# Kernel optimization log

Measured on AMD Instinct MI355X. Metric: run time of the kernel, lower is better.

The kernel has to match this reference:

```python
import jax, jax.numpy as jnp
import numpy as np

EPS = 1e-5  # torch GroupNorm default


def setup_inputs() -> dict:
    key = jax.random.key(0)
    ks = jax.random.split(key, 6)
    C = 256
    B, F, H, W = 1, 8, 32, 32
    scale = 1.0 / np.sqrt(C)  # keep logits well-scaled
    return {
        "x": jax.random.normal(ks[0], (B, C, F, H, W), dtype=jnp.float32),
        "gn_w": jnp.ones((C,), jnp.float32),
        "gn_b": jnp.zeros((C,), jnp.float32),
        "qw": jax.random.normal(ks[1], (C, C), jnp.float32) * scale,
        "qb": jnp.zeros((C,), jnp.float32),
        "kw": jax.random.normal(ks[2], (C, C), jnp.float32) * scale,
        "kb": jnp.zeros((C,), jnp.float32),
        "vw": jax.random.normal(ks[3], (C, C), jnp.float32) * scale,
        "vb": jnp.zeros((C,), jnp.float32),
        "ow": jax.random.normal(ks[4], (C, C), jnp.float32) * scale,
        "ob": jnp.zeros((C,), jnp.float32),
    }


def reference(x, gn_w, gn_b, qw, qb, kw, kb, vw, vb, ow, ob):
    B, C, F, H, W = x.shape
    N = F * H * W
    # GroupNorm(1, C): normalize over (C,F,H,W) per sample, per-channel affine
    mean = jnp.mean(x, axis=(1, 2, 3, 4), keepdims=True)
    var = jnp.var(x, axis=(1, 2, 3, 4), keepdims=True)
    xn = (x - mean) * jax.lax.rsqrt(var + EPS)
    xn = xn * gn_w[None, :, None, None, None] + gn_b[None, :, None, None, None]
    xf = xn.reshape(B, C, N)  # [B, C, N]
    # 1x1x1 Conv3d == channel matmul
    q = jnp.einsum('oc,bcn->bon', qw, xf) + qb[None, :, None]
    k = jnp.einsum('oc,bcn->bon', kw, xf) + kb[None, :, None]
    v = jnp.einsum('oc,bcn->bon', vw, xf) + vb[None, :, None]
    # scores[b, n_q, n_k] = q^T k, scaled by C^-0.5
    scores = jnp.einsum('bcn,bcm->bnm', q, k) * (C ** -0.5)
    weights = jax.nn.softmax(scores, axis=-1)  # over keys
    # attention[b, c, n_q] = sum_m v[b,c,m] * weights[b,n_q,m]
    att = jnp.einsum('bcm,bnm->bcn', v, weights)
    att = jnp.einsum('oc,bcn->bon', ow, att) + ob[None, :, None]
    return xn + att.reshape(B, C, F, H, W)
```

## Files before the change

### kernel.cpp

```cpp
#include <hip/hip_runtime.h>
#include <hip/hip_bf16.h>
#include <cstdint>

#define NSP 8192
#define CCH 256
#define KBLK 32
#define NSPLIT 8
#define KEYS_PER_SPLIT 1024
#define NTILES 32

typedef __attribute__((ext_vector_type(4))) float f32x4;
typedef __attribute__((ext_vector_type(16))) float f32x16;
typedef __attribute__((ext_vector_type(8))) short bf16x8;
typedef __attribute__((ext_vector_type(2))) unsigned int u32x2;

__device__ __forceinline__ ushort f2bf(float f) {
  union { float f; uint32_t u; } v; v.f = f;
  uint32_t r = (v.u + 0x7FFFu + ((v.u >> 16) & 1u)) >> 16;
  return (ushort)r;
}
__device__ __forceinline__ float bf2f(ushort u) {
  union { uint32_t u; float f; } v; v.u = ((uint32_t)u) << 16; return v.f;
}
__device__ __forceinline__ uint32_t pk2bf(float lo, float hi) {
  __hip_bfloat162 h = __float22bfloat162_rn({lo, hi});
  union { __hip_bfloat162 h; uint32_t u; } c; c.h = h; return c.u;
}

__device__ __forceinline__ void gload_lds16(const void* g, void* l) {
  auto gp = (const __attribute__((address_space(1))) uint32_t*)(uintptr_t)g;
  auto lp = (__attribute__((address_space(3))) uint32_t*)(uint32_t)(uintptr_t)l;
  __builtin_amdgcn_global_load_lds(gp, lp, 16, 0, 0);
}

__device__ __forceinline__ void perm32swap(uint32_t& a, uint32_t& b) {
#if __has_builtin(__builtin_amdgcn_permlane32_swap)
  u32x2 r = __builtin_amdgcn_permlane32_swap(a, b, false, false);
  a = r[0]; b = r[1];
#else
  uint32_t sa = __shfl_xor((int)a, 32), sb = __shfl_xor((int)b, 32);
  bool lo = (threadIdx.x & 63) < 32;
  uint32_t na = lo ? a : sb;
  uint32_t nb = lo ? sa : b;
  a = na; b = nb;
#endif
}

__global__ __launch_bounds__(256) void k_stats1(const float* __restrict__ x,
                                                float* __restrict__ part) {
  int t = threadIdx.x, b = blockIdx.x;
  float s = 0.f, ss = 0.f;
  const float4* x4 = (const float4*)x;
  for (int i = 0; i < 4; ++i) {
    float4 v = x4[(size_t)i * 131072 + b * 256 + t];
    s += v.x + v.y + v.z + v.w;
    ss += v.x * v.x + v.y * v.y + v.z * v.z + v.w * v.w;
  }
  for (int m = 1; m < 64; m <<= 1) { s += __shfl_xor(s, m); ss += __shfl_xor(ss, m); }
  __shared__ float ls[4], lss[4];
  int w = t >> 6, lane = t & 63;
  if (lane == 0) { ls[w] = s; lss[w] = ss; }
  __syncthreads();
  if (t == 0) {
    part[b * 2 + 0] = ls[0] + ls[1] + ls[2] + ls[3];
    part[b * 2 + 1] = lss[0] + lss[1] + lss[2] + lss[3];
  }
}

__global__ __launch_bounds__(256) void k_castw(const float* __restrict__ qw, const float* __restrict__ kw,
                                               const float* __restrict__ vw, const float* __restrict__ ow,
                                               ushort* __restrict__ wqkv, ushort* __restrict__ wo,
                                               const float* __restrict__ part, float* __restrict__ stat) {
  if (blockIdx.x == 1024) {
    int t = threadIdx.x;
    float s = 0.f, ss = 0.f;
    for (int i = t; i < 512; i += 256) { s += part[i * 2]; ss += part[i * 2 + 1]; }
    for (int m = 1; m < 64; m <<= 1) { s += __shfl_xor(s, m); ss += __shfl_xor(ss, m); }
    __shared__ float ls[4], lss[4];
    int w = t >> 6, lane = t & 63;
    if (lane == 0) { ls[w] = s; lss[w] = ss; }
    __syncthreads();
    if (t == 0) {
      float sum = ls[0] + ls[1] + ls[2] + ls[3];
      float ssum = lss[0] + lss[1] + lss[2] + lss[3];
      float mean = sum * (1.f / 2097152.f);
      float var = ssum * (1.f / 2097152.f) - mean * mean;
      stat[0] = mean;
      stat[1] = rsqrtf(var + 1e-5f);
    }
    return;
  }
  int idx = blockIdx.x * 256 + threadIdx.x;
  if (idx < 65536) wqkv[idx] = f2bf(qw[idx]);
  else if (idx < 131072) wqkv[idx] = f2bf(kw[idx - 65536]);
  else if (idx < 196608) wqkv[idx] = f2bf(vw[idx - 131072]);
  else wo[idx - 196608] = f2bf(ow[idx - 196608]);
}

__global__ __launch_bounds__(256) void k_norm_t(const float* __restrict__ x,
                                                const float* __restrict__ gw, const float* __restrict__ gb,
                                                const float* __restrict__ stat, ushort* __restrict__ xnT) {
  __shared__ float tile[64][66];
  int n0 = blockIdx.x * 64, c0 = blockIdx.y * 64;
  int t = threadIdx.x, colr = t & 63, rq = t >> 6;
  float mean = stat[0], rinv = stat[1];
  for (int rr = 0; rr < 16; ++rr) {
    int row = rr * 4 + rq;
    int c = c0 + row;
    float v = x[(size_t)c * NSP + n0 + colr];
    tile[row][colr] = (v - mean) * rinv * gw[c] + gb[c];
  }
  __syncthreads();
  for (int rr = 0; rr < 16; ++rr) {
    int rowW = rr * 4 + rq;
    xnT[(size_t)(n0 + rowW) * 256 + c0 + colr] = f2bf(tile[colr][rowW]);
  }
}

__global__ __launch_bounds__(256) void k_qkv(const ushort* __restrict__ xnT, const ushort* __restrict__ wqkv,
                                             const float* __restrict__ qb, const float* __restrict__ kb,
                                             const float* __restrict__ vb,
                                             ushort* __restrict__ qT, ushort* __restrict__ kT,
                                             ushort* __restrict__ v_tiles) {
  __shared__ ushort tile[64][80];
  int nb = blockIdx.x, ob = blockIdx.y;
  int w = threadIdx.x >> 6, lane = threadIdx.x & 63;
  int l16 = lane & 15, kgrp = lane >> 4;
  int n_row = nb * 64 + w * 16 + l16;
  bf16x8 a[8];
  const bf16x8* arow = (const bf16x8*)(xnT + (size_t)n_row * 256);
  for (int ks = 0; ks < 8; ++ks) a[ks] = arow[ks * 4 + kgrp];
  f32x4 acc[4];
  for (int ct = 0; ct < 4; ++ct) {
    int o = ob * 64 + ct * 16 + l16;
    const bf16x8* brow = (const bf16x8*)(wqkv + (size_t)o * 256);
    f32x4 c = {0.f, 0.f, 0.f, 0.f};
    for (int ks = 0; ks < 8; ++ks)
      c = __builtin_amdgcn_mfma_f32_16x16x32_bf16(a[ks], brow[ks * 4 + kgrp], c, 0, 0, 0);
    acc[ct] = c;
  }
  const float SCALE = 0.0625f * 1.44269504088896340736f;
  if (ob < 8) {
    for (int ct = 0; ct < 4; ++ct) {
      int o = ob * 64 + ct * 16 + l16;
      for (int r = 0; r < 4; ++r) {
        int n = nb * 64 + w * 16 + kgrp * 4 + r;
        float v = acc[ct][r];
        if (o < 256) qT[(size_t)n * 256 + o] = f2bf((v + qb[o]) * SCALE);
        else kT[(size_t)n * 256 + (o - 256)] = f2bf(v + kb[o - 256]);
      }
    }
  } else {
    for (int ct = 0; ct < 4; ++ct) {
      int o_l = ct * 16 + l16;
      for (int r = 0; r < 4; ++r) {
        int n_l = w * 16 + kgrp * 4 + r;
        tile[o_l][n_l] = f2bf(acc[ct][r] + vb[(ob - 8) * 64 + o_l]);
      }
    }
    __syncthreads();
    for (int j = 0; j < 2; ++j) {
      int idx = j * 256 + threadIdx.x;
      int tile_l = idx >> 8, slot = (idx >> 6) & 3, c_l = idx & 63;
      size_t off = (size_t)(nb * 2 + tile_l) * 8192 + slot * 2048 +
                   (size_t)((ob - 8) * 64 + c_l) * 8;
      *(uint4*)((char*)v_tiles + off * 2) = *(const uint4*)&tile[c_l][tile_l * 32 + slot * 8];
    }
  }
}

__global__ __launch_bounds__(512, 2) void k_attn(const ushort* __restrict__ qT, const ushort* __restrict__ kT,
                                                 const ushort* __restrict__ v_tiles,
                                                 ushort* __restrict__ Opart, float* __restrict__ mpart,
                                                 float* __restrict__ lpart) {
  __shared__ __align__(16) ushort SMEM[32768];
  ushort* k_lds = SMEM;
  ushort* v_lds = SMEM + 16384;

  int bid = blockIdx.x;
  int split = bid & 7, qblk = bid >> 3;
  int t = threadIdx.x, w = t >> 6, lane = t & 63;
  int l31 = lane & 31, lhi = lane >> 5, l7 = lane & 7;
  int q0w = qblk * 256 + w * 32;

  bf16x8 qf[16];
  {
    const char* qbase = (const char*)qT + (size_t)(q0w + l31) * 512;
#pragma unroll
    for (int cs = 0; cs < 16; ++cs)
      qf[cs] = *(const bf16x8*)(qbase + cs * 32 + lhi * 16);
  }

  f32x16 acc[8] = {};
  float m_r = -1e30f, l_p = 0.f;
  bf16x8 pf0, pf1;

  const char* kT_b = (const char*)kT + (size_t)split * KEYS_PER_SPLIT * 512;
  const char* v_b = (const char*)v_tiles + (size_t)split * KEYS_PER_SPLIT * 512;

  auto STAGE_K = [&](int tt) {
    const char* ksrc = kT_b + (size_t)tt * KBLK * 512;
    char* kdst = (char*)(k_lds + (tt & 1) * 8192) + w * 2048;
#pragma unroll
    for (int i = 0; i < 2; ++i) {
      int keyloc = w * 4 + i * 2 + lhi;
      int srcoff = keyloc * 512 + ((l31 ^ (keyloc & 7)) << 4);
      gload_lds16(ksrc + srcoff, kdst + i * 1024);
    }
  };
  auto STAGE_V = [&](int tt) {
    char* vdst = (char*)(v_lds + (tt & 1) * 8192) + w * 2048;
    const char* vsrc = v_b + (size_t)tt * 16384 + w * 2048;
#pragma unroll
    for (int i = 0; i < 2; ++i)
      gload_lds16(vsrc + i * 1024 + lane * 16, vdst + i * 1024);
  };

  auto SOFTMAX_PACK = [&](f32x16& S0) {
    float x0 = fmaxf(S0[0], S0[1]), x1 = fmaxf(S0[2], S0[3]);
    float x2 = fmaxf(S0[4], S0[5]), x3 = fmaxf(S0[6], S0[7]);
    float x4 = fmaxf(S0[8], S0[9]), x5 = fmaxf(S0[10], S0[11]);
    float x6 = fmaxf(S0[12], S0[13]), x7 = fmaxf(S0[14], S0[15]);
    float pm = fmaxf(fmaxf(fmaxf(x0, x1), fmaxf(x2, x3)),
                     fmaxf(fmaxf(x4, x5), fmaxf(x6, x7)));
    pm = fmaxf(pm, __shfl_xor(pm, 32));
    if (!__all(pm <= m_r + 8.f)) {
      float mn = fmaxf(m_r, pm);
      float alpha = __builtin_amdgcn_exp2f(m_r - mn);
      m_r = mn;
      l_p *= alpha;
#pragma unroll
      for (int cb = 0; cb < 8; ++cb)
#pragma unroll
        for (int r = 0; r < 16; ++r) acc[cb][r] *= alpha;
    }
    {
      float t0s = 0.f, t1s = 0.f, t2s = 0.f, t3s = 0.f;
#pragma unroll
      for (int r = 0; r < 16; ++r) {
        S0[r] = __builtin_amdgcn_exp2f(S0[r] - m_r);
        if (r < 4) t0s += S0[r];
        else if (r < 8) t1s += S0[r];
        else if (r < 12) t2s += S0[r];
        else t3s += S0[r];
      }
      l_p += (t0s + t1s) + (t2s + t3s);
    }
    union { uint32_t w[4]; bf16x8 v; } u;
    {
      uint32_t x = pk2bf(S0[0], S0[1]), y = pk2bf(S0[4], S0[5]);
      perm32swap(x, y);
      uint32_t x2_ = pk2bf(S0[2], S0[3]), y2 = pk2bf(S0[6], S0[7]);
      perm32swap(x2_, y2);
      u.w[0] = x; u.w[1] = x2_; u.w[2] = y; u.w[3] = y2;
      pf0 = u.v;
    }
    {
      uint32_t x = pk2bf(S0[8], S0[9]), y = pk2bf(S0[12], S0[13]);
      perm32swap(x, y);
      uint32_t x2_ = pk2bf(S0[10], S0[11]), y2 = pk2bf(S0[14], S0[15]);
      perm32swap(x2_, y2);
      u.w[0] = x; u.w[1] = x2_; u.w[2] = y; u.w[3] = y2;
      pf1 = u.v;
    }
  };

  STAGE_K(0);

  asm volatile("s_waitcnt vmcnt(0) lgkmcnt(0)" ::: "memory");
  __builtin_amdgcn_s_barrier();
  __builtin_amdgcn_sched_barrier(0);
  STAGE_K(1);
  STAGE_V(0);
  {
    const ushort* kl = k_lds;
    f32x16 S0 = {};
    __builtin_amdgcn_s_setprio(1);
#pragma unroll
    for (int cs = 0; cs < 16; ++cs) {
      int slot = (cs * 2 + lhi) ^ l7;
      bf16x8 a0 = *(const bf16x8*)(kl + l31 * 256 + slot * 8);
      S0 = __builtin_amdgcn_mfma_f32_32x32x16_bf16(a0, qf[cs], S0, 0, 0, 0);
    }
    __builtin_amdgcn_s_setprio(0);
    SOFTMAX_PACK(S0);
  }

#pragma unroll 1
  for (int tt = 1; tt < NTILES; ++tt) {
    asm volatile("s_waitcnt vmcnt(0) lgkmcnt(0)" ::: "memory");
    __builtin_amdgcn_s_barrier();
    __builtin_amdgcn_sched_barrier(0);
    if (tt + 1 < NTILES) STAGE_K(tt + 1);
    STAGE_V(tt);

    const ushort* kl = k_lds + (tt & 1) * 8192;
    const ushort* vl = v_lds + ((tt - 1) & 1) * 8192;
    f32x16 S0 = {};
    __builtin_amdgcn_s_setprio(1);
#pragma unroll
    for (int cb = 0; cb < 8; ++cb) {
      bf16x8 va0 = *(const bf16x8*)(vl + (0 + lhi) * 2048 + (cb * 32 + l31) * 8);
      acc[cb] = __builtin_amdgcn_mfma_f32_32x32x16_bf16(va0, pf0, acc[cb], 0, 0, 0);
      {
        int cs = 2 * cb;
        int slot = (cs * 2 + lhi) ^ l7;
        bf16x8 ka = *(const bf16x8*)(kl + l31 * 256 + slot * 8);
        S0 = __builtin_amdgcn_mfma_f32_32x32x16_bf16(ka, qf[cs], S0, 0, 0, 0);
      }
      bf16x8 va1 = *(const bf16x8*)(vl + (2 + lhi) * 2048 + (cb * 32 + l31) * 8);
      acc[cb] = __builtin_amdgcn_mfma_f32_32x32x16_bf16(va1, pf1, acc[cb], 0, 0, 0);
      {
        int cs = 2 * cb + 1;
        int slot = (cs * 2 + lhi) ^ l7;
        bf16x8 ka = *(const bf16x8*)(kl + l31 * 256 + slot * 8);
        S0 = __builtin_amdgcn_mfma_f32_32x32x16_bf16(ka, qf[cs], S0, 0, 0, 0);
      }
    }
    __builtin_amdgcn_s_setprio(0);
    SOFTMAX_PACK(S0);
  }

  asm volatile("s_waitcnt vmcnt(0) lgkmcnt(0)" ::: "memory");
  __builtin_amdgcn_s_barrier();
  {
    const ushort* vl = v_lds + ((NTILES - 1) & 1) * 8192;
    __builtin_amdgcn_s_setprio(1);
#pragma unroll
    for (int cb = 0; cb < 8; ++cb) {
      bf16x8 va0 = *(const bf16x8*)(vl + (0 + lhi) * 2048 + (cb * 32 + l31) * 8);
      acc[cb] = __builtin_amdgcn_mfma_f32_32x32x16_bf16(va0, pf0, acc[cb], 0, 0, 0);
      bf16x8 va1 = *(const bf16x8*)(vl + (2 + lhi) * 2048 + (cb * 32 + l31) * 8);
      acc[cb] = __builtin_amdgcn_mfma_f32_32x32x16_bf16(va1, pf1, acc[cb], 0, 0, 0);
    }
    __builtin_amdgcn_s_setprio(0);
  }

  asm volatile("s_waitcnt lgkmcnt(0)" ::: "memory");
  __builtin_amdgcn_s_barrier();

  float l_tot = l_p + __shfl_xor(l_p, 32);

  char* eb = (char*)SMEM + w * 4608;
  size_t gq0 = (size_t)split * NSP + q0w;
#pragma unroll
  for (int ch = 0; ch < 4; ++ch) {
#pragma unroll
    for (int cb2 = 0; cb2 < 2; ++cb2) {
      int cb = ch * 2 + cb2;
#pragma unroll
      for (int g = 0; g < 4; ++g) {
        int cl = cb2 * 32 + g * 8 + 4 * lhi;
        *(uint32_t*)(eb + l31 * 144 + cl * 2) = pk2bf(acc[cb][g * 4 + 0], acc[cb][g * 4 + 1]);
        *(uint32_t*)(eb + l31 * 144 + cl * 2 + 4) = pk2bf(acc[cb][g * 4 + 2], acc[cb][g * 4 + 3]);
      }
    }
    asm volatile("s_waitcnt lgkmcnt(0)" ::: "memory");
    __builtin_amdgcn_sched_barrier(0);
#pragma unroll
    for (int i = 0; i < 4; ++i) {
      int flat = i * 1024 + lane * 16;
      int qr = flat >> 7, off = flat & 127;
      uint4 val = *(const uint4*)(eb + qr * 144 + off);
      *(uint4*)((char*)Opart + (gq0 + qr) * 512 + ch * 128 + off) = val;
    }
    asm volatile("s_waitcnt lgkmcnt(0)" ::: "memory");
    __builtin_amdgcn_sched_barrier(0);
  }
  if (lane < 32) {
    int q = q0w + l31;
    mpart[split * NSP + q] = m_r;
    lpart[split * NSP + q] = l_tot;
  }
}

__global__ __launch_bounds__(256) void k_combine(const ushort* __restrict__ Opart,
                                                 const float* __restrict__ mpart,
                                                 const float* __restrict__ lpart,
                                                 ushort* __restrict__ attT) {
  int q = blockIdx.x * 8 + (threadIdx.x >> 5);
  int c8 = threadIdx.x & 31;
  float M = -1e30f;
#pragma unroll
  for (int s = 0; s < NSPLIT; ++s) M = fmaxf(M, mpart[s * NSP + q]);
  float L = 0.f;
  float av[8] = {};
#pragma unroll
  for (int s = 0; s < NSPLIT; ++s) {
    float ws = __builtin_amdgcn_exp2f(mpart[s * NSP + q] - M);
    L += ws * lpart[s * NSP + q];
    bf16x8 o = *(const bf16x8*)(Opart + ((size_t)s * NSP + q) * 256 + c8 * 8);
#pragma unroll
    for (int j = 0; j < 8; ++j) av[j] += ws * bf2f((ushort)o[j]);
  }
  float rL = 1.f / L;
  uint4 outv;
  outv.x = pk2bf(av[0] * rL, av[1] * rL);
  outv.y = pk2bf(av[2] * rL, av[3] * rL);
  outv.z = pk2bf(av[4] * rL, av[5] * rL);
  outv.w = pk2bf(av[6] * rL, av[7] * rL);
  *(uint4*)(attT + (size_t)q * 256 + c8 * 8) = outv;
}

__global__ __launch_bounds__(256) void k_final(const ushort* __restrict__ attT, const ushort* __restrict__ wo,
                                               const float* __restrict__ ob, const float* __restrict__ x,
                                               const float* __restrict__ gw, const float* __restrict__ gb,
                                               const float* __restrict__ stat, float* __restrict__ out) {
  int nb = blockIdx.x, obk = blockIdx.y;
  int w = threadIdx.x >> 6, lane = threadIdx.x & 63;
  int l16 = lane & 15, kgrp = lane >> 4;
  int orow = obk * 64 + w * 16 + l16;
  bf16x8 a[8];
  const bf16x8* arow = (const bf16x8*)(wo + (size_t)orow * 256);
  for (int ks = 0; ks < 8; ++ks) a[ks] = arow[ks * 4 + kgrp];
  float mean = stat[0], rinv = stat[1];
  f32x4 acc[4];
  for (int ct = 0; ct < 4; ++ct) {
    int n = nb * 64 + ct * 16 + l16;
    const bf16x8* brow = (const bf16x8*)(attT + (size_t)n * 256);
    f32x4 c = {0.f, 0.f, 0.f, 0.f};
    for (int ks = 0; ks < 8; ++ks)
      c = __builtin_amdgcn_mfma_f32_16x16x32_bf16(a[ks], brow[ks * 4 + kgrp], c, 0, 0, 0);
    acc[ct] = c;
  }
  for (int ct = 0; ct < 4; ++ct) {
    for (int r = 0; r < 4; ++r) {
      int o = obk * 64 + w * 16 + kgrp * 4 + r;
      int n = nb * 64 + ct * 16 + l16;
      float xv = x[(size_t)o * NSP + n];
      float xn = (xv - mean) * rinv * gw[o] + gb[o];
      out[(size_t)o * NSP + n] = xn + acc[ct][r] + ob[o];
    }
  }
}

extern "C" void kernel_launch(void* const* d_in, const int* in_sizes, int n_in,
                              void* d_out, int out_size, void* d_ws, size_t ws_size,
                              hipStream_t stream) {
  const float* x = (const float*)d_in[0];
  const float* gw = (const float*)d_in[1];
  const float* gb = (const float*)d_in[2];
  const float* qw = (const float*)d_in[3];
  const float* qbv = (const float*)d_in[4];
  const float* kw = (const float*)d_in[5];
  const float* kbv = (const float*)d_in[6];
  const float* vw = (const float*)d_in[7];
  const float* vbv = (const float*)d_in[8];
  const float* ow = (const float*)d_in[9];
  const float* obv = (const float*)d_in[10];
  float* out = (float*)d_out;
  char* ws = (char*)d_ws;
  const size_t KB = 1024, MB = 1048576;
  float* part = (float*)(ws);
  float* stat = (float*)(ws + 60 * KB);
  ushort* wqkv = (ushort*)(ws + 64 * KB);
  ushort* wo = (ushort*)(ws + 448 * KB);
  float* mpart = (float*)(ws + 64 * KB);
  float* lpart = (float*)(ws + 576 * KB);
  ushort* xnT = (ushort*)(ws + 1 * MB);
  ushort* qT = (ushort*)(ws + 5 * MB);
  ushort* kT = (ushort*)(ws + 9 * MB);
  ushort* v_tiles = (ushort*)(ws + 13 * MB);
  ushort* Opart = (ushort*)(ws + 17 * MB);
  ushort* attT = xnT;

  k_stats1<<<512, 256, 0, stream>>>(x, part);
  k_castw<<<1025, 256, 0, stream>>>(qw, kw, vw, ow, wqkv, wo, part, stat);
  k_norm_t<<<dim3(128, 4), 256, 0, stream>>>(x, gw, gb, stat, xnT);
  k_qkv<<<dim3(128, 12), 256, 0, stream>>>(xnT, wqkv, qbv, kbv, vbv, qT, kT, v_tiles);
  k_attn<<<256, 512, 0, stream>>>(qT, kT, v_tiles, Opart, mpart, lpart);
  k_combine<<<NSP / 8, 256, 0, stream>>>(Opart, mpart, lpart, attT);
  k_final<<<dim3(128, 4), 256, 0, stream>>>(attT, wo, obv, x, gw, gb, stat, out);
}
```

Measured before the change: 135.5 us.

## Pre-tile K in QKV kernel to remove LDS XOR swizzle in attention

The QKV projection now writes K into a pre-tiled layout through an LDS transpose, so each 32-key tile is stored as 8-element channel slots laid out contiguously across keys. The attention kernel can then stage K with fully contiguous per-lane loads and read its MFMA operands without the XOR-swizzle address math. The aim is cheaper address computation and bank-conflict-free LDS reads in the inner loop. The cost is an extra LDS transpose and sync in the K-producing blocks of the QKV kernel.

```diff
diff --git a/kernel.cpp b/kernel.cpp
--- a/kernel.cpp
+++ b/kernel.cpp
@@ -120,7 +120,7 @@
 __global__ __launch_bounds__(256) void k_qkv(const ushort* __restrict__ xnT, const ushort* __restrict__ wqkv,
                                              const float* __restrict__ qb, const float* __restrict__ kb,
                                              const float* __restrict__ vb,
-                                             ushort* __restrict__ qT, ushort* __restrict__ kT,
+                                             ushort* __restrict__ qT, ushort* __restrict__ k_tiles,
                                              ushort* __restrict__ v_tiles) {
   __shared__ ushort tile[64][80];
   int nb = blockIdx.x, ob = blockIdx.y;
@@ -140,15 +140,29 @@
     acc[ct] = c;
   }
   const float SCALE = 0.0625f * 1.44269504088896340736f;
-  if (ob < 8) {
+  if (ob < 4) {
     for (int ct = 0; ct < 4; ++ct) {
       int o = ob * 64 + ct * 16 + l16;
       for (int r = 0; r < 4; ++r) {
         int n = nb * 64 + w * 16 + kgrp * 4 + r;
-        float v = acc[ct][r];
-        if (o < 256) qT[(size_t)n * 256 + o] = f2bf((v + qb[o]) * SCALE);
-        else kT[(size_t)n * 256 + (o - 256)] = f2bf(v + kb[o - 256]);
-      }
+        qT[(size_t)n * 256 + o] = f2bf((acc[ct][r] + qb[o]) * SCALE);
+      }
+    }
+  } else if (ob < 8) {
+    for (int ct = 0; ct < 4; ++ct) {
+      int o_l = ct * 16 + l16;
+      for (int r = 0; r < 4; ++r) {
+        int n_l = w * 16 + kgrp * 4 + r;
+        tile[n_l][o_l] = f2bf(acc[ct][r] + kb[(ob - 4) * 64 + o_l]);
+      }
+    }
+    __syncthreads();
+    for (int j = 0; j < 2; ++j) {
+      int idx = j * 256 + threadIdx.x;
+      int tile_l = idx >> 8, s = (idx >> 5) & 7, key = idx & 31;
+      size_t off = (size_t)(nb * 2 + tile_l) * 16384 +
+                   (size_t)((ob - 4) * 8 + s) * 512 + key * 16;
+      *(uint4*)((char*)k_tiles + off) = *(const uint4*)&tile[tile_l * 32 + key][s * 8];
     }
   } else {
     for (int ct = 0; ct < 4; ++ct) {
@@ -169,7 +183,7 @@
   }
 }
 
-__global__ __launch_bounds__(512, 2) void k_attn(const ushort* __restrict__ qT, const ushort* __restrict__ kT,
+__global__ __launch_bounds__(512, 2) void k_attn(const ushort* __restrict__ qT, const ushort* __restrict__ k_tiles,
                                                  const ushort* __restrict__ v_tiles,
                                                  ushort* __restrict__ Opart, float* __restrict__ mpart,
                                                  float* __restrict__ lpart) {
@@ -180,7 +194,7 @@
   int bid = blockIdx.x;
   int split = bid & 7, qblk = bid >> 3;
   int t = threadIdx.x, w = t >> 6, lane = t & 63;
-  int l31 = lane & 31, lhi = lane >> 5, l7 = lane & 7;
+  int l31 = lane & 31, lhi = lane >> 5;
   int q0w = qblk * 256 + w * 32;
 
   bf16x8 qf[16];
@@ -195,18 +209,15 @@
   float m_r = -1e30f, l_p = 0.f;
   bf16x8 pf0, pf1;
 
-  const char* kT_b = (const char*)kT + (size_t)split * KEYS_PER_SPLIT * 512;
+  const char* kT_b = (const char*)k_tiles + (size_t)split * KEYS_PER_SPLIT * 512;
   const char* v_b = (const char*)v_tiles + (size_t)split * KEYS_PER_SPLIT * 512;
 
   auto STAGE_K = [&](int tt) {
-    const char* ksrc = kT_b + (size_t)tt * KBLK * 512;
+    const char* ksrc = kT_b + (size_t)tt * 16384 + w * 2048;
     char* kdst = (char*)(k_lds + (tt & 1) * 8192) + w * 2048;
 #pragma unroll
-    for (int i = 0; i < 2; ++i) {
-      int keyloc = w * 4 + i * 2 + lhi;
-      int srcoff = keyloc * 512 + ((l31 ^ (keyloc & 7)) << 4);
-      gload_lds16(ksrc + srcoff, kdst + i * 1024);
-    }
+    for (int i = 0; i < 2; ++i)
+      gload_lds16(ksrc + i * 1024 + lane * 16, kdst + i * 1024);
   };
   auto STAGE_V = [&](int tt) {
     char* vdst = (char*)(v_lds + (tt & 1) * 8192) + w * 2048;
@@ -278,8 +289,8 @@
     __builtin_amdgcn_s_setprio(1);
 #pragma unroll
     for (int cs = 0; cs < 16; ++cs) {
-      int slot = (cs * 2 + lhi) ^ l7;
-      bf16x8 a0 = *(const bf16x8*)(kl + l31 * 256 + slot * 8);
+      int slot = cs * 2 + lhi;
+      bf16x8 a0 = *(const bf16x8*)(kl + slot * 256 + l31 * 8);
       S0 = __builtin_amdgcn_mfma_f32_32x32x16_bf16(a0, qf[cs], S0, 0, 0, 0);
     }
     __builtin_amdgcn_s_setprio(0);
@@ -303,18 +314,16 @@
       bf16x8 va0 = *(const bf16x8*)(vl + (0 + lhi) * 2048 + (cb * 32 + l31) * 8);
       acc[cb] = __builtin_amdgcn_mfma_f32_32x32x16_bf16(va0, pf0, acc[cb], 0, 0, 0);
       {
-        int cs = 2 * cb;
-        int slot = (cs * 2 + lhi) ^ l7;
-        bf16x8 ka = *(const bf16x8*)(kl + l31 * 256 + slot * 8);
-        S0 = __builtin_amdgcn_mfma_f32_32x32x16_bf16(ka, qf[cs], S0, 0, 0, 0);
+        int slot = 4 * cb + lhi;
+        bf16x8 ka = *(const bf16x8*)(kl + slot * 256 + l31 * 8);
+        S0 = __builtin_amdgcn_mfma_f32_32x32x16_bf16(ka, qf[2 * cb], S0, 0, 0, 0);
       }
       bf16x8 va1 = *(const bf16x8*)(vl + (2 + lhi) * 2048 + (cb * 32 + l31) * 8);
       acc[cb] = __builtin_amdgcn_mfma_f32_32x32x16_bf16(va1, pf1, acc[cb], 0, 0, 0);
       {
-        int cs = 2 * cb + 1;
-        int slot = (cs * 2 + lhi) ^ l7;
-        bf16x8 ka = *(const bf16x8*)(kl + l31 * 256 + slot * 8);
-        S0 = __builtin_amdgcn_mfma_f32_32x32x16_bf16(ka, qf[cs], S0, 0, 0, 0);
+        int slot = 4 * cb + 2 + lhi;
+        bf16x8 ka = *(const bf16x8*)(kl + slot * 256 + l31 * 8);
+        S0 = __builtin_amdgcn_mfma_f32_32x32x16_bf16(ka, qf[2 * cb + 1], S0, 0, 0, 0);
       }
     }
     __builtin_amdgcn_s_setprio(0);
@@ -459,7 +468,7 @@
   float* lpart = (float*)(ws + 576 * KB);
   ushort* xnT = (ushort*)(ws + 1 * MB);
   ushort* qT = (ushort*)(ws + 5 * MB);
-  ushort* kT = (ushort*)(ws + 9 * MB);
+  ushort* k_tiles = (ushort*)(ws + 9 * MB);
   ushort* v_tiles = (ushort*)(ws + 13 * MB);
   ushort* Opart = (ushort*)(ws + 17 * MB);
   ushort* attT = xnT;
@@ -467,8 +476,8 @@
   k_stats1<<<512, 256, 0, stream>>>(x, part);
   k_castw<<<1025, 256, 0, stream>>>(qw, kw, vw, ow, wqkv, wo, part, stat);
   k_norm_t<<<dim3(128, 4), 256, 0, stream>>>(x, gw, gb, stat, xnT);
-  k_qkv<<<dim3(128, 12), 256, 0, stream>>>(xnT, wqkv, qbv, kbv, vbv, qT, kT, v_tiles);
-  k_attn<<<256, 512, 0, stream>>>(qT, kT, v_tiles, Opart, mpart, lpart);
+  k_qkv<<<dim3(128, 12), 256, 0, stream>>>(xnT, wqkv, qbv, kbv, vbv, qT, k_tiles, v_tiles);
+  k_attn<<<256, 512, 0, stream>>>(qT, k_tiles, v_tiles, Opart, mpart, lpart);
   k_combine<<<NSP / 8, 256, 0, stream>>>(Opart, mpart, lpart, attT);
   k_final<<<dim3(128, 4), 256, 0, stream>>>(attT, wo, obv, x, gw, gb, stat, out);
 }
```

Result: no change. 133.8 us (-1.3%).
